# Performance work log

Measured on AMD Instinct MI355X. Metric: run time of the kernel, lower is better.

## Reference

```python
import jax, jax.numpy as jnp
import numpy as np

D_MODEL = 768
CTX_DIM = 1024
N_HEAD = 12
N_QUERIES = 256
DIM_HEAD = D_MODEL // N_HEAD  # 64
INNER = DIM_HEAD * N_HEAD     # 768
EPS = 1e-5


def layernorm(x, w, b):
    mu = jnp.mean(x, axis=-1, keepdims=True)
    var = jnp.mean((x - mu) ** 2, axis=-1, keepdims=True)
    return (x - mu) * jax.lax.rsqrt(var + EPS) * w + b


def setup_inputs() -> dict:
    key = jax.random.key(0)
    ks = jax.random.split(key, 9)
    x = jax.random.normal(ks[0], (8, 4096, CTX_DIM), dtype=jnp.float32)
    query = jax.random.normal(ks[1], (N_QUERIES, D_MODEL), dtype=jnp.float32)
    # Linear weights stored [in, out] (y = x @ W)
    Wq = jax.random.normal(ks[2], (D_MODEL, INNER), dtype=jnp.float32) * 0.02
    Wkv = jax.random.normal(ks[3], (CTX_DIM, 2 * INNER), dtype=jnp.float32) * 0.02
    Wout = jax.random.normal(ks[4], (INNER, D_MODEL), dtype=jnp.float32) * 0.02
    ln_q_w = jnp.ones((D_MODEL,), jnp.float32)
    ln_q_b = jnp.zeros((D_MODEL,), jnp.float32)
    ln_k_w = jnp.ones((CTX_DIM,), jnp.float32)
    ln_k_b = jnp.zeros((CTX_DIM,), jnp.float32)
    return {"x": x, "query": query, "ln_q_w": ln_q_w, "ln_q_b": ln_q_b,
            "ln_k_w": ln_k_w, "ln_k_b": ln_k_b, "Wq": Wq, "Wkv": Wkv, "Wout": Wout}


def reference(x, query, ln_q_w, ln_q_b, ln_k_w, ln_k_b, Wq, Wkv, Wout):
    b = x.shape[0]
    h, dh = N_HEAD, DIM_HEAD
    scale = dh ** -0.5
    xk = x[:, None]  # b 1 n d  (m = 1)
    m, n = xk.shape[1], xk.shape[2]
    q = jnp.broadcast_to(query, (b, m) + query.shape)  # b m nq d
    xk = layernorm(xk, ln_k_w, ln_k_b)
    q = layernorm(q, ln_q_w, ln_q_b)
    q = q @ Wq                          # b m nq inner
    kv = xk @ Wkv                       # b m n 2*inner
    k, v = jnp.split(kv, 2, axis=-1)
    def split_heads(t):
        bb, tt, nn, _ = t.shape
        return t.reshape(bb, tt, nn, h, dh).transpose(0, 3, 1, 2, 4)  # b h t n dh
    q, k, v = split_heads(q), split_heads(k), split_heads(v)
    sim = jnp.einsum('bhtid,bhtjd->bhtij', q * scale, k)
    attn = jax.nn.softmax(sim, axis=-1)
    out = jnp.einsum('bhtij,bhtjd->bhtid', attn, v)  # b h t nq dh
    out = out.transpose(0, 2, 3, 1, 4).reshape(b, m, N_QUERIES, INNER)
    return (out @ Wout).squeeze(axis=1)  # b nq d_model
```

## Files before the change

### kernel.cpp

```cpp
#include <hip/hip_runtime.h>
#include <hip/hip_bf16.h>
#include <math.h>

#define B_    8
#define T_    4096
#define CD    1024
#define DM    768
#define NH    12
#define DH    64
#define NQ    256
#define INNER 768
#define NKV   1536
#define MKV   (B_*T_)
#define EPS   1e-5f
#define SCALE 0.125f

typedef __attribute__((ext_vector_type(8))) short short8;
typedef __attribute__((ext_vector_type(4))) float f32x4;

__device__ __forceinline__ unsigned short f2bf(float f) {
  union { __hip_bfloat16 h; unsigned short u; } cv;
  cv.h = __float2bfloat16(f);
  return cv.u;
}

__global__ __launch_bounds__(256) void tb32_kernel(
    const float* __restrict__ src, unsigned short* __restrict__ dst,
    int Cn, int R) {
  __shared__ float tile[32][33];
  int k0 = blockIdx.x * 32, n0 = blockIdx.y * 32;
  int tid = threadIdx.x;
  int r = tid >> 3, c4 = (tid & 7) * 4;
  float4 v = *reinterpret_cast<const float4*>(&src[(size_t)(k0 + r) * Cn + n0 + c4]);
  tile[r][c4 + 0] = v.x; tile[r][c4 + 1] = v.y; tile[r][c4 + 2] = v.z; tile[r][c4 + 3] = v.w;
  __syncthreads();
  ushort4 o4;
  o4.x = f2bf(tile[c4 + 0][r]);
  o4.y = f2bf(tile[c4 + 1][r]);
  o4.z = f2bf(tile[c4 + 2][r]);
  o4.w = f2bf(tile[c4 + 3][r]);
  *reinterpret_cast<ushort4*>(&dst[(size_t)(n0 + r) * R + k0 + c4]) = o4;
}

__global__ __launch_bounds__(256) void qln_kernel(
    const float* __restrict__ query, const float* __restrict__ lnw,
    const float* __restrict__ lnb, unsigned short* __restrict__ qn) {
  int row = blockIdx.x, tid = threadIdx.x;
  __shared__ float rbuf[256];
  const float* qr = query + (size_t)row * DM;
  float v0 = qr[tid], v1 = qr[tid + 256], v2 = qr[tid + 512];
  rbuf[tid] = v0 + v1 + v2;
  __syncthreads();
  for (int o = 128; o > 0; o >>= 1) { if (tid < o) rbuf[tid] += rbuf[tid + o]; __syncthreads(); }
  float mean = rbuf[0] * (1.f / 768.f);
  __syncthreads();
  float d0 = v0 - mean, d1 = v1 - mean, d2 = v2 - mean;
  rbuf[tid] = d0 * d0 + d1 * d1 + d2 * d2;
  __syncthreads();
  for (int o = 128; o > 0; o >>= 1) { if (tid < o) rbuf[tid] += rbuf[tid + o]; __syncthreads(); }
  float var = rbuf[0] * (1.f / 768.f);
  float rs = rsqrtf(var + EPS);
  unsigned short* dst = qn + (size_t)row * DM;
  dst[tid]       = f2bf(d0 * rs * lnw[tid]       + lnb[tid]);
  dst[tid + 256] = f2bf(d1 * rs * lnw[tid + 256] + lnb[tid + 256]);
  dst[tid + 512] = f2bf(d2 * rs * lnw[tid + 512] + lnb[tid + 512]);
}

__global__ __launch_bounds__(256) void xnorm_kernel(
    const float* __restrict__ x, const float* __restrict__ lnw,
    const float* __restrict__ lnb, unsigned short* __restrict__ xn) {
  int row = blockIdx.x, tid = threadIdx.x;
  float4 v = reinterpret_cast<const float4*>(x + (size_t)row * CD)[tid];
  float s  = v.x + v.y + v.z + v.w;
  float ss = v.x * v.x + v.y * v.y + v.z * v.z + v.w * v.w;
  #pragma unroll
  for (int o = 32; o > 0; o >>= 1) { s += __shfl_down(s, o); ss += __shfl_down(ss, o); }
  __shared__ float sm[8];
  int wid = tid >> 6, lane = tid & 63;
  if (lane == 0) { sm[wid] = s; sm[4 + wid] = ss; }
  __syncthreads();
  float S  = sm[0] + sm[1] + sm[2] + sm[3];
  float SS = sm[4] + sm[5] + sm[6] + sm[7];
  float m  = S * (1.f / 1024.f);
  float var = SS * (1.f / 1024.f) - m * m;
  float rs = rsqrtf(fmaxf(var, 0.f) + EPS);
  float4 wv = reinterpret_cast<const float4*>(lnw)[tid];
  float4 bv = reinterpret_cast<const float4*>(lnb)[tid];
  ushort4 o4;
  o4.x = f2bf((v.x - m) * rs * wv.x + bv.x);
  o4.y = f2bf((v.y - m) * rs * wv.y + bv.y);
  o4.z = f2bf((v.z - m) * rs * wv.z + bv.z);
  o4.w = f2bf((v.w - m) * rs * wv.w + bv.w);
  reinterpret_cast<ushort4*>(xn + (size_t)row * CD)[tid] = o4;
}

template <int MODE>
__global__ __launch_bounds__(256) void gemm128_kernel(
    const unsigned short* __restrict__ A, const unsigned short* __restrict__ Bt,
    void* __restrict__ Cout, int N, int K, int nN, float scale, int swz) {
  __shared__ __attribute__((aligned(16))) unsigned short As[128 * 64];
  __shared__ __attribute__((aligned(16))) unsigned short Bs[128 * 64];
  int tid = threadIdx.x;
  int w = tid >> 6, lane = tid & 63;
  int bid = blockIdx.x;
  int sw = swz ? ((bid & 7) * ((int)gridDim.x >> 3) + (bid >> 3)) : bid;
  int mt = sw / nN, nt = sw % nN;
  int m0 = mt * 128, n0 = nt * 128;

  int srow[4], skoff[4];
  #pragma unroll
  for (int i = 0; i < 4; ++i) {
    int L = w * 4096 + i * 1024 + lane * 16;
    int row = L >> 7;
    int slot = (L >> 4) & 7;
    srow[i] = row;
    skoff[i] = ((slot ^ (row & 7)) << 3);
  }

  f32x4 acc[4][4];
  #pragma unroll
  for (int m = 0; m < 4; ++m)
    #pragma unroll
    for (int n = 0; n < 4; ++n) acc[m][n] = (f32x4){0.f, 0.f, 0.f, 0.f};

  int wr = w >> 1, wc = w & 1;
  int l15 = lane & 15, l4 = lane >> 4;

  for (int t = 0; t < K / 64; ++t) {
    int k0 = t * 64;
    #pragma unroll
    for (int i = 0; i < 4; ++i) {
      __builtin_amdgcn_global_load_lds(
          (const __attribute__((address_space(1))) void*)(A + (size_t)(m0 + srow[i]) * K + k0 + skoff[i]),
          (__attribute__((address_space(3))) void*)(As + w * 2048 + i * 512 + lane * 8),
          16, 0, 0);
    }
    #pragma unroll
    for (int i = 0; i < 4; ++i) {
      __builtin_amdgcn_global_load_lds(
          (const __attribute__((address_space(1))) void*)(Bt + (size_t)(n0 + srow[i]) * K + k0 + skoff[i]),
          (__attribute__((address_space(3))) void*)(Bs + w * 2048 + i * 512 + lane * 8),
          16, 0, 0);
    }
    __syncthreads();
    #pragma unroll
    for (int kh = 0; kh < 2; ++kh) {
      short8 af[4], bf[4];
      #pragma unroll
      for (int m = 0; m < 4; ++m) {
        int row = wr * 64 + m * 16 + l15;
        int byte = row * 128 + (((l4 + 4 * kh) ^ (row & 7)) << 4);
        af[m] = *reinterpret_cast<const short8*>(reinterpret_cast<const char*>(As) + byte);
      }
      #pragma unroll
      for (int n = 0; n < 4; ++n) {
        int row = wc * 64 + n * 16 + l15;
        int byte = row * 128 + (((l4 + 4 * kh) ^ (row & 7)) << 4);
        bf[n] = *reinterpret_cast<const short8*>(reinterpret_cast<const char*>(Bs) + byte);
      }
      #pragma unroll
      for (int m = 0; m < 4; ++m)
        #pragma unroll
        for (int n = 0; n < 4; ++n)
          acc[m][n] = __builtin_amdgcn_mfma_f32_16x16x32_bf16(af[m], bf[n], acc[m][n], 0, 0, 0);
    }
    __syncthreads();
  }

  #pragma unroll
  for (int m = 0; m < 4; ++m) {
    int grow = m0 + wr * 64 + m * 16 + l4 * 4;
    #pragma unroll
    for (int n = 0; n < 4; ++n) {
      int gcol = n0 + wc * 64 + n * 16 + l15;
      #pragma unroll
      for (int r = 0; r < 4; ++r) {
        if (MODE == 0)
          ((unsigned short*)Cout)[(size_t)(grow + r) * N + gcol] = f2bf(acc[m][n][r] * scale);
        else
          ((float*)Cout)[(size_t)(grow + r) * N + gcol] = acc[m][n][r];
      }
    }
  }
}

#define KBM 256
#define KBN 256
#define KBK 64
__global__ __launch_bounds__(512, 2) void kv_mfma256_kernel(
    const unsigned short* __restrict__ xn, const unsigned short* __restrict__ wkvT,
    unsigned short* __restrict__ kvb) {
  __shared__ __attribute__((aligned(16))) unsigned short As[2][KBM * KBK];
  __shared__ __attribute__((aligned(16))) unsigned short Bs[2][KBN * KBK];
  int tid = threadIdx.x;
  int w = tid >> 6, lane = tid & 63;
  int wm = w >> 2, wn = w & 3;
  int l15 = lane & 15, l4 = lane >> 4;

  int bid = blockIdx.x;
  int sw = (bid & 7) * 96 + (bid >> 3);
  int mt = sw / (NKV / KBN), nt = sw % (NKV / KBN);
  int m0 = mt * KBM, n0 = nt * KBN;

  int srow[4], koff[4];
  #pragma unroll
  for (int i = 0; i < 4; ++i) {
    int r = i * 64 + (tid >> 3);
    srow[i] = r;
    koff[i] = (((tid & 7) ^ (r & 7)) << 3);
  }

  f32x4 acc[8][4];
  #pragma unroll
  for (int m = 0; m < 8; ++m)
    #pragma unroll
    for (int n = 0; n < 4; ++n) acc[m][n] = (f32x4){0.f, 0.f, 0.f, 0.f};

  #pragma unroll
  for (int i = 0; i < 4; ++i) {
    __builtin_amdgcn_global_load_lds(
        (const __attribute__((address_space(1))) void*)(xn + (size_t)(m0 + srow[i]) * CD + koff[i]),
        (__attribute__((address_space(3))) void*)(&As[0][0] + i * 4096 + tid * 8), 16, 0, 0);
    __builtin_amdgcn_global_load_lds(
        (const __attribute__((address_space(1))) void*)(wkvT + (size_t)(n0 + srow[i]) * CD + koff[i]),
        (__attribute__((address_space(3))) void*)(&Bs[0][0] + i * 4096 + tid * 8), 16, 0, 0);
  }
  __syncthreads();

  for (int t = 0; t < CD / KBK; ++t) {
    int cur = t & 1;
    if (t + 1 < CD / KBK) {
      int k0 = (t + 1) * KBK;
      #pragma unroll
      for (int i = 0; i < 4; ++i) {
        __builtin_amdgcn_global_load_lds(
            (const __attribute__((address_space(1))) void*)(xn + (size_t)(m0 + srow[i]) * CD + k0 + koff[i]),
            (__attribute__((address_space(3))) void*)(&As[cur ^ 1][0] + i * 4096 + tid * 8), 16, 0, 0);
        __builtin_amdgcn_global_load_lds(
            (const __attribute__((address_space(1))) void*)(wkvT + (size_t)(n0 + srow[i]) * CD + k0 + koff[i]),
            (__attribute__((address_space(3))) void*)(&Bs[cur ^ 1][0] + i * 4096 + tid * 8), 16, 0, 0);
      }
    }
    const char* Ab = reinterpret_cast<const char*>(&As[cur][0]);
    const char* Bb = reinterpret_cast<const char*>(&Bs[cur][0]);
    #pragma unroll
    for (int kh = 0; kh < 2; ++kh) {
      short8 bf[4];
      #pragma unroll
      for (int n = 0; n < 4; ++n) {
        int row = wn * 64 + n * 16 + l15;
        int byt = row * 128 + (((kh * 4 + l4) ^ (row & 7)) << 4);
        bf[n] = *reinterpret_cast<const short8*>(Bb + byt);
      }
      #pragma unroll
      for (int m = 0; m < 8; ++m) {
        int row = wm * 128 + m * 16 + l15;
        int byt = row * 128 + (((kh * 4 + l4) ^ (row & 7)) << 4);
        short8 af = *reinterpret_cast<const short8*>(Ab + byt);
        #pragma unroll
        for (int n = 0; n < 4; ++n)
          acc[m][n] = __builtin_amdgcn_mfma_f32_16x16x32_bf16(af, bf[n], acc[m][n], 0, 0, 0);
      }
    }
    __syncthreads();
  }

  #pragma unroll
  for (int m = 0; m < 8; ++m) {
    int grow = m0 + wm * 128 + m * 16 + l4 * 4;
    #pragma unroll
    for (int n = 0; n < 4; ++n) {
      int gcol = n0 + wn * 64 + n * 16 + l15;
      #pragma unroll
      for (int r = 0; r < 4; ++r)
        kvb[(size_t)(grow + r) * NKV + gcol] = f2bf(acc[m][n][r]);
    }
  }
}

__global__ __launch_bounds__(256) void vtrans_kernel(
    const unsigned short* __restrict__ kvb, unsigned short* __restrict__ vT) {
  int jt = blockIdx.x, bh = blockIdx.y;
  int b = bh / NH, h = bh % NH;
  __shared__ __attribute__((aligned(16))) unsigned short t_[64][72];
  int tid = threadIdx.x;
  {
    int jr = tid >> 2, dp = (tid & 3) * 16;
    const unsigned short* src = kvb + (size_t)(b * T_ + jt * 64 + jr) * NKV + INNER + h * DH + dp;
    *reinterpret_cast<short8*>(&t_[jr][dp])     = *reinterpret_cast<const short8*>(src);
    *reinterpret_cast<short8*>(&t_[jr][dp + 8]) = *reinterpret_cast<const short8*>(src + 8);
  }
  __syncthreads();
  {
    int d = tid >> 2, jp = (tid & 3) * 16;
    unsigned short tmp[16];
    #pragma unroll
    for (int jj = 0; jj < 16; ++jj) tmp[jj] = t_[jp + jj][d];
    unsigned short* dst = vT + ((size_t)bh * DH + d) * T_ + jt * 64 + jp;
    *reinterpret_cast<short8*>(dst)     = *reinterpret_cast<const short8*>(&tmp[0]);
    *reinterpret_cast<short8*>(dst + 8) = *reinterpret_cast<const short8*>(&tmp[8]);
  }
}

__global__ __launch_bounds__(256) void attn_mfma_kernel(
    const unsigned short* __restrict__ qpb, const unsigned short* __restrict__ kvb,
    const unsigned short* __restrict__ vT,
    float* __restrict__ pO, float* __restrict__ pM, float* __restrict__ pL) {
  int qt = blockIdx.x, kc = blockIdx.y, bh = blockIdx.z;
  int b = bh / NH, h = bh % NH;
  __shared__ __attribute__((aligned(16))) unsigned short Ks[4096];
  __shared__ __attribute__((aligned(16))) unsigned short Vs[4096];
  __shared__ __attribute__((aligned(16))) unsigned short Ps[4][1024];
  int tid = threadIdx.x;
  int w = tid >> 6, lane = tid & 63;
  int l15 = lane & 15, l4 = lane >> 4;

  short8 qf[2];
  {
    const unsigned short* qb = qpb + (size_t)(qt * 64 + w * 16 + l15) * INNER + h * DH;
    qf[0] = *reinterpret_cast<const short8*>(qb + l4 * 8);
    qf[1] = *reinterpret_cast<const short8*>(qb + 32 + l4 * 8);
  }

  int srow0 = w * 16 + (lane >> 3);
  int srow1 = srow0 + 8;
  int koff0 = (((lane & 7) ^ (srow0 & 7)) << 3);
  int koff1 = (((lane & 7) ^ (srow1 & 7)) << 3);

  f32x4 o[4];
  #pragma unroll
  for (int i = 0; i < 4; ++i) o[i] = (f32x4){0.f, 0.f, 0.f, 0.f};
  float m_run = -1e30f, l_run = 0.f;

  const size_t kbase = ((size_t)b * T_) * NKV + h * DH;
  const size_t vbase = ((size_t)bh * DH) * T_;

  for (int kt = 0; kt < 32; ++kt) {
    int j0 = kc * 2048 + kt * 64;
    __builtin_amdgcn_global_load_lds(
        (const __attribute__((address_space(1))) void*)(kvb + kbase + (size_t)(j0 + srow0) * NKV + koff0),
        (__attribute__((address_space(3))) void*)(Ks + w * 1024 + lane * 8), 16, 0, 0);
    __builtin_amdgcn_global_load_lds(
        (const __attribute__((address_space(1))) void*)(kvb + kbase + (size_t)(j0 + srow1) * NKV + koff1),
        (__attribute__((address_space(3))) void*)(Ks + w * 1024 + 512 + lane * 8), 16, 0, 0);
    __builtin_amdgcn_global_load_lds(
        (const __attribute__((address_space(1))) void*)(vT + vbase + (size_t)srow0 * T_ + j0 + koff0),
        (__attribute__((address_space(3))) void*)(Vs + w * 1024 + lane * 8), 16, 0, 0);
    __builtin_amdgcn_global_load_lds(
        (const __attribute__((address_space(1))) void*)(vT + vbase + (size_t)srow1 * T_ + j0 + koff1),
        (__attribute__((address_space(3))) void*)(Vs + w * 1024 + 512 + lane * 8), 16, 0, 0);
    __syncthreads();

    f32x4 st[4];
    #pragma unroll
    for (int sub = 0; sub < 4; ++sub) {
      st[sub] = (f32x4){0.f, 0.f, 0.f, 0.f};
      #pragma unroll
      for (int hf = 0; hf < 2; ++hf) {
        int row = sub * 16 + l15;
        int byt = row * 128 + (((l4 + 4 * hf) ^ (row & 7)) << 4);
        short8 kf = *reinterpret_cast<const short8*>(reinterpret_cast<const char*>(Ks) + byt);
        st[sub] = __builtin_amdgcn_mfma_f32_16x16x32_bf16(kf, qf[hf], st[sub], 0, 0, 0);
      }
    }

    float tmax = -1e30f;
    #pragma unroll
    for (int sub = 0; sub < 4; ++sub)
      #pragma unroll
      for (int r = 0; r < 4; ++r) tmax = fmaxf(tmax, st[sub][r]);
    tmax = fmaxf(tmax, __shfl_xor(tmax, 16));
    tmax = fmaxf(tmax, __shfl_xor(tmax, 32));
    float m_new = fmaxf(m_run, tmax);
    float alpha = __expf(m_run - m_new);
    float psum = 0.f;
    #pragma unroll
    for (int sub = 0; sub < 4; ++sub) {
      float p0 = __expf(st[sub][0] - m_new);
      float p1 = __expf(st[sub][1] - m_new);
      float p2 = __expf(st[sub][2] - m_new);
      float p3 = __expf(st[sub][3] - m_new);
      psum += (p0 + p1) + (p2 + p3);
      unsigned int u0 = (unsigned int)f2bf(p0) | ((unsigned int)f2bf(p1) << 16);
      unsigned int u1 = (unsigned int)f2bf(p2) | ((unsigned int)f2bf(p3) << 16);
      int slot = (sub * 2 + (l4 >> 1)) ^ (l15 & 7);
      int byt = l15 * 128 + (slot << 4) + (l4 & 1) * 8;
      uint2 uv; uv.x = u0; uv.y = u1;
      *reinterpret_cast<uint2*>(reinterpret_cast<char*>(Ps[w]) + byt) = uv;
    }
    psum += __shfl_xor(psum, 16);
    psum += __shfl_xor(psum, 32);
    l_run = l_run * alpha + psum;
    m_run = m_new;

    float ao[4];
    #pragma unroll
    for (int r = 0; r < 4; ++r) ao[r] = __shfl(alpha, (l4 << 2) | r);
    #pragma unroll
    for (int ds = 0; ds < 4; ++ds)
      #pragma unroll
      for (int r = 0; r < 4; ++r) o[ds][r] *= ao[r];

    short8 pa[2];
    #pragma unroll
    for (int hf = 0; hf < 2; ++hf) {
      int byt = l15 * 128 + ((((hf << 2) + l4) ^ (l15 & 7)) << 4);
      pa[hf] = *reinterpret_cast<const short8*>(reinterpret_cast<const char*>(Ps[w]) + byt);
    }
    #pragma unroll
    for (int ds = 0; ds < 4; ++ds) {
      #pragma unroll
      for (int hf = 0; hf < 2; ++hf) {
        int row = ds * 16 + l15;
        int byt = row * 128 + (((l4 + 4 * hf) ^ (row & 7)) << 4);
        short8 vf = *reinterpret_cast<const short8*>(reinterpret_cast<const char*>(Vs) + byt);
        o[ds] = __builtin_amdgcn_mfma_f32_16x16x32_bf16(pa[hf], vf, o[ds], 0, 0, 0);
      }
    }
    __syncthreads();
  }

  int pidx = bh * 2 + kc;
  int qrow0 = qt * 64 + w * 16;
  if (l4 == 0) {
    pM[(size_t)pidx * NQ + qrow0 + l15] = m_run;
    pL[(size_t)pidx * NQ + qrow0 + l15] = l_run;
  }
  #pragma unroll
  for (int ds = 0; ds < 4; ++ds)
    #pragma unroll
    for (int r = 0; r < 4; ++r)
      pO[((size_t)pidx * NQ + qrow0 + l4 * 4 + r) * DH + ds * 16 + l15] = o[ds][r];
}

__global__ __launch_bounds__(256) void attn_combine_kernel(
    const float* __restrict__ pO, const float* __restrict__ pM,
    const float* __restrict__ pL, unsigned short* __restrict__ attn_out) {
  int qt = blockIdx.x, bh = blockIdx.y;
  int b = bh / NH, h = bh % NH;
  int tid = threadIdx.x;
  #pragma unroll
  for (int e = 0; e < 16; ++e) {
    int idx = e * 256 + tid;
    int r = idx >> 6, d = idx & 63;
    int row = qt * 64 + r;
    size_t i0 = (size_t)(bh * 2 + 0) * NQ + row;
    size_t i1 = (size_t)(bh * 2 + 1) * NQ + row;
    float m1 = pM[i0], m2 = pM[i1], l1 = pL[i0], l2 = pL[i1];
    float M = fmaxf(m1, m2);
    float w1 = __expf(m1 - M), w2 = __expf(m2 - M);
    float L = l1 * w1 + l2 * w2;
    float oo = (pO[i0 * DH + d] * w1 + pO[i1 * DH + d] * w2) / L;
    attn_out[((size_t)b * NQ + row) * INNER + h * DH + d] = f2bf(oo);
  }
}

extern "C" void kernel_launch(void* const* d_in, const int* in_sizes, int n_in,
                              void* d_out, int out_size, void* d_ws, size_t ws_size,
                              hipStream_t stream) {
  const float* x      = (const float*)d_in[0];
  const float* query  = (const float*)d_in[1];
  const float* ln_q_w = (const float*)d_in[2];
  const float* ln_q_b = (const float*)d_in[3];
  const float* ln_k_w = (const float*)d_in[4];
  const float* ln_k_b = (const float*)d_in[5];
  const float* Wq     = (const float*)d_in[6];
  const float* Wkv    = (const float*)d_in[7];
  const float* Wout   = (const float*)d_in[8];
  float* out = (float*)d_out;

  unsigned short* qpb   = (unsigned short*)d_ws;
  unsigned short* xn    = qpb + (size_t)NQ * INNER;
  unsigned short* vT    = xn;
  unsigned short* wkvT  = xn + (size_t)MKV * CD;
  unsigned short* kvb   = wkvT + (size_t)NKV * CD;
  float* pO    = (float*)(kvb + (size_t)MKV * NKV);
  float* pM    = pO + (size_t)B_ * NH * 2 * NQ * DH;
  float* pL    = pM + (size_t)B_ * NH * 2 * NQ;
  unsigned short* attnb = (unsigned short*)(pL + (size_t)B_ * NH * 2 * NQ);
  unsigned short* qn    = attnb + (size_t)B_ * NQ * INNER;
  unsigned short* WqT   = qn + (size_t)NQ * DM;
  unsigned short* WoutT = WqT + (size_t)DM * INNER;

  hipLaunchKernelGGL(tb32_kernel, dim3(CD / 32, NKV / 32), dim3(256), 0, stream,
                     Wkv, wkvT, NKV, CD);
  hipLaunchKernelGGL(tb32_kernel, dim3(DM / 32, INNER / 32), dim3(256), 0, stream,
                     Wq, WqT, INNER, DM);
  hipLaunchKernelGGL(tb32_kernel, dim3(INNER / 32, DM / 32), dim3(256), 0, stream,
                     Wout, WoutT, DM, INNER);
  hipLaunchKernelGGL(qln_kernel, dim3(NQ), dim3(256), 0, stream,
                     query, ln_q_w, ln_q_b, qn);
  hipLaunchKernelGGL((gemm128_kernel<0>), dim3((NQ / 128) * (INNER / 128)), dim3(256), 0, stream,
                     qn, WqT, (void*)qpb, INNER, DM, INNER / 128, SCALE, 0);
  hipLaunchKernelGGL(xnorm_kernel, dim3(MKV), dim3(256), 0, stream,
                     x, ln_k_w, ln_k_b, xn);
  hipLaunchKernelGGL(kv_mfma256_kernel, dim3((MKV / KBM) * (NKV / KBN)), dim3(512), 0, stream,
                     xn, wkvT, kvb);
  hipLaunchKernelGGL(vtrans_kernel, dim3(T_ / 64, B_ * NH), dim3(256), 0, stream,
                     kvb, vT);
  hipLaunchKernelGGL(attn_mfma_kernel, dim3(4, 2, B_ * NH), dim3(256), 0, stream,
                     qpb, kvb, vT, pO, pM, pL);
  hipLaunchKernelGGL(attn_combine_kernel, dim3(4, B_ * NH), dim3(256), 0, stream,
                     pO, pM, pL, attnb);
  hipLaunchKernelGGL((gemm128_kernel<1>), dim3((B_ * NQ / 128) * (DM / 128)), dim3(256), 0, stream,
                     attnb, WoutT, (void*)out, DM, INNER, DM / 128, 1.f, 1);
}
```

Baseline: 284.8 us.

## Restructure KV GEMM into quadrant-phased 8-wave pipeline with split staging

Rewrites the KV projection GEMM so each K-step is split into four MFMA quadrants. Each half-tile of A and B is staged separately and interleaved between the quadrants, with fine-grained vmcnt waits and s_barriers. The goal is to overlap global-to-LDS loads with MFMA work and raise MFMA issue priority with s_setprio, replacing the single whole-tile prefetch plus __syncthreads. setprio is also added around the MFMA blocks in the attention kernel. The many extra barriers and the tighter hand scheduling risk stalls, and the vmcnt counting could be fragile.

```diff
diff --git a/kernel.cpp b/kernel.cpp
--- a/kernel.cpp
+++ b/kernel.cpp
@@ -187,11 +187,31 @@
 #define KBM 256
 #define KBN 256
 #define KBK 64
-__global__ __launch_bounds__(512, 2) void kv_mfma256_kernel(
+#define NT  (CD / KBK)
+
+#define QUAD(qm, qn)                                                          \
+  do {                                                                        \
+    __builtin_amdgcn_s_setprio(1);                                            \
+    _Pragma("unroll")                                                         \
+    for (int m_ = 0; m_ < 4; ++m_) {                                          \
+      _Pragma("unroll")                                                       \
+      for (int n_ = 0; n_ < 2; ++n_) {                                        \
+        acc[(qm)*4 + m_][(qn)*2 + n_] = __builtin_amdgcn_mfma_f32_16x16x32_bf16( \
+            areg[(qm)*4 + m_][0], breg[(qn)*2 + n_][0],                       \
+            acc[(qm)*4 + m_][(qn)*2 + n_], 0, 0, 0);                          \
+        acc[(qm)*4 + m_][(qn)*2 + n_] = __builtin_amdgcn_mfma_f32_16x16x32_bf16( \
+            areg[(qm)*4 + m_][1], breg[(qn)*2 + n_][1],                       \
+            acc[(qm)*4 + m_][(qn)*2 + n_], 0, 0, 0);                          \
+      }                                                                       \
+    }                                                                         \
+    __builtin_amdgcn_s_setprio(0);                                            \
+  } while (0)
+
+__global__ __launch_bounds__(512, 2) void kv_mfma8p_kernel(
     const unsigned short* __restrict__ xn, const unsigned short* __restrict__ wkvT,
     unsigned short* __restrict__ kvb) {
-  __shared__ __attribute__((aligned(16))) unsigned short As[2][KBM * KBK];
-  __shared__ __attribute__((aligned(16))) unsigned short Bs[2][KBN * KBK];
+  __shared__ __attribute__((aligned(16))) unsigned short AsL[2][2][128 * 64];
+  __shared__ __attribute__((aligned(16))) unsigned short BsL[2][2][128 * 64];
   int tid = threadIdx.x;
   int w = tid >> 6, lane = tid & 63;
   int wm = w >> 2, wn = w & 3;
@@ -202,13 +222,31 @@
   int mt = sw / (NKV / KBN), nt = sw % (NKV / KBN);
   int m0 = mt * KBM, n0 = nt * KBN;
 
-  int srow[4], koff[4];
-  #pragma unroll
-  for (int i = 0; i < 4; ++i) {
-    int r = i * 64 + (tid >> 3);
-    srow[i] = r;
-    koff[i] = (((tid & 7) ^ (r & 7)) << 3);
-  }
+  int sr0 = tid >> 3;
+  int sr1 = 64 + (tid >> 3);
+  int sk0 = ((tid & 7) ^ (sr0 & 7)) << 3;
+  int sk1 = ((tid & 7) ^ (sr1 & 7)) << 3;
+
+  auto stageA = [&](int t, int h) {
+    int d = t & 1;
+    const unsigned short* src = xn + (size_t)(m0 + h * 128) * CD + t * KBK;
+    __builtin_amdgcn_global_load_lds(
+        (const __attribute__((address_space(1))) void*)(src + (size_t)sr0 * CD + sk0),
+        (__attribute__((address_space(3))) void*)(&AsL[d][h][0] + tid * 8), 16, 0, 0);
+    __builtin_amdgcn_global_load_lds(
+        (const __attribute__((address_space(1))) void*)(src + (size_t)sr1 * CD + sk1),
+        (__attribute__((address_space(3))) void*)(&AsL[d][h][4096] + tid * 8), 16, 0, 0);
+  };
+  auto stageB = [&](int t, int h) {
+    int d = t & 1;
+    const unsigned short* src = wkvT + (size_t)(n0 + h * 128) * CD + t * KBK;
+    __builtin_amdgcn_global_load_lds(
+        (const __attribute__((address_space(1))) void*)(src + (size_t)sr0 * CD + sk0),
+        (__attribute__((address_space(3))) void*)(&BsL[d][h][0] + tid * 8), 16, 0, 0);
+    __builtin_amdgcn_global_load_lds(
+        (const __attribute__((address_space(1))) void*)(src + (size_t)sr1 * CD + sk1),
+        (__attribute__((address_space(3))) void*)(&BsL[d][h][4096] + tid * 8), 16, 0, 0);
+  };
 
   f32x4 acc[8][4];
   #pragma unroll
@@ -216,53 +254,56 @@
     #pragma unroll
     for (int n = 0; n < 4; ++n) acc[m][n] = (f32x4){0.f, 0.f, 0.f, 0.f};
 
-  #pragma unroll
-  for (int i = 0; i < 4; ++i) {
-    __builtin_amdgcn_global_load_lds(
-        (const __attribute__((address_space(1))) void*)(xn + (size_t)(m0 + srow[i]) * CD + koff[i]),
-        (__attribute__((address_space(3))) void*)(&As[0][0] + i * 4096 + tid * 8), 16, 0, 0);
-    __builtin_amdgcn_global_load_lds(
-        (const __attribute__((address_space(1))) void*)(wkvT + (size_t)(n0 + srow[i]) * CD + koff[i]),
-        (__attribute__((address_space(3))) void*)(&Bs[0][0] + i * 4096 + tid * 8), 16, 0, 0);
-  }
-  __syncthreads();
-
-  for (int t = 0; t < CD / KBK; ++t) {
-    int cur = t & 1;
-    if (t + 1 < CD / KBK) {
-      int k0 = (t + 1) * KBK;
-      #pragma unroll
-      for (int i = 0; i < 4; ++i) {
-        __builtin_amdgcn_global_load_lds(
-            (const __attribute__((address_space(1))) void*)(xn + (size_t)(m0 + srow[i]) * CD + k0 + koff[i]),
-            (__attribute__((address_space(3))) void*)(&As[cur ^ 1][0] + i * 4096 + tid * 8), 16, 0, 0);
-        __builtin_amdgcn_global_load_lds(
-            (const __attribute__((address_space(1))) void*)(wkvT + (size_t)(n0 + srow[i]) * CD + k0 + koff[i]),
-            (__attribute__((address_space(3))) void*)(&Bs[cur ^ 1][0] + i * 4096 + tid * 8), 16, 0, 0);
-      }
-    }
-    const char* Ab = reinterpret_cast<const char*>(&As[cur][0]);
-    const char* Bb = reinterpret_cast<const char*>(&Bs[cur][0]);
-    #pragma unroll
-    for (int kh = 0; kh < 2; ++kh) {
-      short8 bf[4];
-      #pragma unroll
-      for (int n = 0; n < 4; ++n) {
-        int row = wn * 64 + n * 16 + l15;
-        int byt = row * 128 + (((kh * 4 + l4) ^ (row & 7)) << 4);
-        bf[n] = *reinterpret_cast<const short8*>(Bb + byt);
-      }
-      #pragma unroll
-      for (int m = 0; m < 8; ++m) {
-        int row = wm * 128 + m * 16 + l15;
-        int byt = row * 128 + (((kh * 4 + l4) ^ (row & 7)) << 4);
-        short8 af = *reinterpret_cast<const short8*>(Ab + byt);
-        #pragma unroll
-        for (int n = 0; n < 4; ++n)
-          acc[m][n] = __builtin_amdgcn_mfma_f32_16x16x32_bf16(af, bf[n], acc[m][n], 0, 0, 0);
-      }
-    }
-    __syncthreads();
+  short8 areg[8][2], breg[4][2];
+
+  auto rdA = [&](int t, int m, int kh) -> short8 {
+    int row = m * 16 + l15;
+    int byt = row * 128 + (((kh * 4 + l4) ^ (row & 7)) << 4);
+    return *reinterpret_cast<const short8*>(
+        reinterpret_cast<const char*>(&AsL[t & 1][wm][0]) + byt);
+  };
+  auto rdB = [&](int t, int n, int kh) -> short8 {
+    int R = wn * 64 + n * 16 + l15;
+    int row = R & 127;
+    int byt = row * 128 + (((kh * 4 + l4) ^ (row & 7)) << 4);
+    return *reinterpret_cast<const short8*>(
+        reinterpret_cast<const char*>(&BsL[t & 1][R >> 7][0]) + byt);
+  };
+
+  stageA(0, 0); stageA(0, 1); stageB(0, 0); stageB(0, 1);
+
+  for (int t = 0; t < NT; ++t) {
+    if (t < NT - 1) {
+      stageA(t + 1, 0);
+      asm volatile("s_waitcnt vmcnt(2)" ::: "memory");
+    } else {
+      asm volatile("s_waitcnt vmcnt(0)" ::: "memory");
+    }
+    __builtin_amdgcn_s_barrier();
+    __builtin_amdgcn_sched_barrier(0);
+    #pragma unroll
+    for (int m = 0; m < 4; ++m) { areg[m][0] = rdA(t, m, 0); areg[m][1] = rdA(t, m, 1); }
+    #pragma unroll
+    for (int n = 0; n < 2; ++n) { breg[n][0] = rdB(t, n, 0); breg[n][1] = rdB(t, n, 1); }
+    QUAD(0, 0);
+    __builtin_amdgcn_s_barrier();
+    if (t < NT - 1) stageA(t + 1, 1);
+    #pragma unroll
+    for (int m = 4; m < 8; ++m) { areg[m][0] = rdA(t, m, 0); areg[m][1] = rdA(t, m, 1); }
+    __builtin_amdgcn_s_barrier();
+    QUAD(1, 0);
+    __builtin_amdgcn_s_barrier();
+    if (t < NT - 1) stageB(t + 1, 0);
+    #pragma unroll
+    for (int n = 2; n < 4; ++n) { breg[n][0] = rdB(t, n, 0); breg[n][1] = rdB(t, n, 1); }
+    __builtin_amdgcn_s_barrier();
+    QUAD(1, 1);
+    __builtin_amdgcn_s_barrier();
+    if (t < NT - 1) stageB(t + 1, 1);
+    __builtin_amdgcn_s_barrier();
+    QUAD(0, 1);
+    __builtin_amdgcn_s_barrier();
+    __builtin_amdgcn_sched_barrier(0);
   }
 
   #pragma unroll
@@ -352,6 +393,7 @@
     __syncthreads();
 
     f32x4 st[4];
+    __builtin_amdgcn_s_setprio(1);
     #pragma unroll
     for (int sub = 0; sub < 4; ++sub) {
       st[sub] = (f32x4){0.f, 0.f, 0.f, 0.f};
@@ -363,6 +405,7 @@
         st[sub] = __builtin_amdgcn_mfma_f32_16x16x32_bf16(kf, qf[hf], st[sub], 0, 0, 0);
       }
     }
+    __builtin_amdgcn_s_setprio(0);
 
     float tmax = -1e30f;
     #pragma unroll
@@ -407,6 +450,7 @@
       int byt = l15 * 128 + ((((hf << 2) + l4) ^ (l15 & 7)) << 4);
       pa[hf] = *reinterpret_cast<const short8*>(reinterpret_cast<const char*>(Ps[w]) + byt);
     }
+    __builtin_amdgcn_s_setprio(1);
     #pragma unroll
     for (int ds = 0; ds < 4; ++ds) {
       #pragma unroll
@@ -417,6 +461,7 @@
         o[ds] = __builtin_amdgcn_mfma_f32_16x16x32_bf16(pa[hf], vf, o[ds], 0, 0, 0);
       }
     }
+    __builtin_amdgcn_s_setprio(0);
     __syncthreads();
   }
 
@@ -494,7 +539,7 @@
                      qn, WqT, (void*)qpb, INNER, DM, INNER / 128, SCALE, 0);
   hipLaunchKernelGGL(xnorm_kernel, dim3(MKV), dim3(256), 0, stream,
                      x, ln_k_w, ln_k_b, xn);
-  hipLaunchKernelGGL(kv_mfma256_kernel, dim3((MKV / KBM) * (NKV / KBN)), dim3(512), 0, stream,
+  hipLaunchKernelGGL(kv_mfma8p_kernel, dim3((MKV / KBM) * (NKV / KBN)), dim3(512), 0, stream,
                      xn, wkvT, kvb);
   hipLaunchKernelGGL(vtrans_kernel, dim3(T_ / 64, B_ * NH), dim3(256), 0, stream,
                      kvb, vT);
```

Result: slower. 314.3 us (+10.4%).

## Use 4-stage LDS ring in KV GEMM and double-buffer K/V in attention

Applied to the files above, without the earlier changes.

The KV projection GEMM moves from a double-buffered K=64 tile to a four-slot ring of K=32 tiles, with three stages prefetched. It waits with explicit vmcnt counts and raw s_barrier, and raises wave priority around the MFMA block. The attention kernel double-buffers its K/V LDS tiles so the next tile's global_load_lds overlaps the current compute instead of stalling on a full sync. The goal is to hide global memory latency behind MFMA work. The hand-written waitcnt counts depend on the exact number of outstanding loads, which is fragile, and the smaller K step doubles barrier frequency in the GEMM.

```diff
diff --git a/kernel.cpp b/kernel.cpp
--- a/kernel.cpp
+++ b/kernel.cpp
@@ -186,12 +186,14 @@
 
 #define KBM 256
 #define KBN 256
-#define KBK 64
-__global__ __launch_bounds__(512, 2) void kv_mfma256_kernel(
+#define RBK 32
+#define RNT (CD / RBK)
+
+__global__ __launch_bounds__(512, 2) void kv_ring_kernel(
     const unsigned short* __restrict__ xn, const unsigned short* __restrict__ wkvT,
     unsigned short* __restrict__ kvb) {
-  __shared__ __attribute__((aligned(16))) unsigned short As[2][KBM * KBK];
-  __shared__ __attribute__((aligned(16))) unsigned short Bs[2][KBN * KBK];
+  __shared__ __attribute__((aligned(16))) unsigned short As[4][KBM * RBK];
+  __shared__ __attribute__((aligned(16))) unsigned short Bs[4][KBN * RBK];
   int tid = threadIdx.x;
   int w = tid >> 6, lane = tid & 63;
   int wm = w >> 2, wn = w & 3;
@@ -202,13 +204,28 @@
   int mt = sw / (NKV / KBN), nt = sw % (NKV / KBN);
   int m0 = mt * KBM, n0 = nt * KBN;
 
-  int srow[4], koff[4];
-  #pragma unroll
-  for (int i = 0; i < 4; ++i) {
-    int r = i * 64 + (tid >> 3);
-    srow[i] = r;
-    koff[i] = (((tid & 7) ^ (r & 7)) << 3);
-  }
+  int sr0 = tid >> 2;
+  int sr1 = 128 + (tid >> 2);
+  int sk0 = ((tid & 3) ^ (sr0 & 3)) << 3;
+  int sk1 = ((tid & 3) ^ (sr1 & 3)) << 3;
+
+  auto stage = [&](int t) {
+    int s = t & 3;
+    const unsigned short* sa = xn + (size_t)m0 * CD + t * RBK;
+    const unsigned short* sb = wkvT + (size_t)n0 * CD + t * RBK;
+    __builtin_amdgcn_global_load_lds(
+        (const __attribute__((address_space(1))) void*)(sa + (size_t)sr0 * CD + sk0),
+        (__attribute__((address_space(3))) void*)(&As[s][0] + tid * 8), 16, 0, 0);
+    __builtin_amdgcn_global_load_lds(
+        (const __attribute__((address_space(1))) void*)(sa + (size_t)sr1 * CD + sk1),
+        (__attribute__((address_space(3))) void*)(&As[s][4096] + tid * 8), 16, 0, 0);
+    __builtin_amdgcn_global_load_lds(
+        (const __attribute__((address_space(1))) void*)(sb + (size_t)sr0 * CD + sk0),
+        (__attribute__((address_space(3))) void*)(&Bs[s][0] + tid * 8), 16, 0, 0);
+    __builtin_amdgcn_global_load_lds(
+        (const __attribute__((address_space(1))) void*)(sb + (size_t)sr1 * CD + sk1),
+        (__attribute__((address_space(3))) void*)(&Bs[s][4096] + tid * 8), 16, 0, 0);
+  };
 
   f32x4 acc[8][4];
   #pragma unroll
@@ -216,53 +233,38 @@
     #pragma unroll
     for (int n = 0; n < 4; ++n) acc[m][n] = (f32x4){0.f, 0.f, 0.f, 0.f};
 
-  #pragma unroll
-  for (int i = 0; i < 4; ++i) {
-    __builtin_amdgcn_global_load_lds(
-        (const __attribute__((address_space(1))) void*)(xn + (size_t)(m0 + srow[i]) * CD + koff[i]),
-        (__attribute__((address_space(3))) void*)(&As[0][0] + i * 4096 + tid * 8), 16, 0, 0);
-    __builtin_amdgcn_global_load_lds(
-        (const __attribute__((address_space(1))) void*)(wkvT + (size_t)(n0 + srow[i]) * CD + koff[i]),
-        (__attribute__((address_space(3))) void*)(&Bs[0][0] + i * 4096 + tid * 8), 16, 0, 0);
-  }
-  __syncthreads();
-
-  for (int t = 0; t < CD / KBK; ++t) {
-    int cur = t & 1;
-    if (t + 1 < CD / KBK) {
-      int k0 = (t + 1) * KBK;
-      #pragma unroll
-      for (int i = 0; i < 4; ++i) {
-        __builtin_amdgcn_global_load_lds(
-            (const __attribute__((address_space(1))) void*)(xn + (size_t)(m0 + srow[i]) * CD + k0 + koff[i]),
-            (__attribute__((address_space(3))) void*)(&As[cur ^ 1][0] + i * 4096 + tid * 8), 16, 0, 0);
-        __builtin_amdgcn_global_load_lds(
-            (const __attribute__((address_space(1))) void*)(wkvT + (size_t)(n0 + srow[i]) * CD + k0 + koff[i]),
-            (__attribute__((address_space(3))) void*)(&Bs[cur ^ 1][0] + i * 4096 + tid * 8), 16, 0, 0);
-      }
-    }
-    const char* Ab = reinterpret_cast<const char*>(&As[cur][0]);
-    const char* Bb = reinterpret_cast<const char*>(&Bs[cur][0]);
-    #pragma unroll
-    for (int kh = 0; kh < 2; ++kh) {
-      short8 bf[4];
-      #pragma unroll
-      for (int n = 0; n < 4; ++n) {
-        int row = wn * 64 + n * 16 + l15;
-        int byt = row * 128 + (((kh * 4 + l4) ^ (row & 7)) << 4);
-        bf[n] = *reinterpret_cast<const short8*>(Bb + byt);
-      }
-      #pragma unroll
-      for (int m = 0; m < 8; ++m) {
-        int row = wm * 128 + m * 16 + l15;
-        int byt = row * 128 + (((kh * 4 + l4) ^ (row & 7)) << 4);
-        short8 af = *reinterpret_cast<const short8*>(Ab + byt);
-        #pragma unroll
-        for (int n = 0; n < 4; ++n)
-          acc[m][n] = __builtin_amdgcn_mfma_f32_16x16x32_bf16(af, bf[n], acc[m][n], 0, 0, 0);
-      }
-    }
-    __syncthreads();
+  stage(0); stage(1); stage(2);
+
+  for (int t = 0; t < RNT; ++t) {
+    if (t + 3 < RNT) stage(t + 3);
+    if (t < RNT - 2)       asm volatile("s_waitcnt vmcnt(8)" ::: "memory");
+    else if (t == RNT - 2) asm volatile("s_waitcnt vmcnt(4)" ::: "memory");
+    else                   asm volatile("s_waitcnt vmcnt(0)" ::: "memory");
+    __builtin_amdgcn_s_barrier();
+    __builtin_amdgcn_sched_barrier(0);
+
+    const char* Ab = reinterpret_cast<const char*>(&As[t & 3][0]);
+    const char* Bb = reinterpret_cast<const char*>(&Bs[t & 3][0]);
+    short8 areg[8], breg[4];
+    #pragma unroll
+    for (int n = 0; n < 4; ++n) {
+      int row = wn * 64 + n * 16 + l15;
+      breg[n] = *reinterpret_cast<const short8*>(Bb + row * 64 + ((l4 ^ (row & 3)) << 4));
+    }
+    #pragma unroll
+    for (int m = 0; m < 8; ++m) {
+      int row = wm * 128 + m * 16 + l15;
+      areg[m] = *reinterpret_cast<const short8*>(Ab + row * 64 + ((l4 ^ (row & 3)) << 4));
+    }
+    __builtin_amdgcn_s_setprio(1);
+    #pragma unroll
+    for (int m = 0; m < 8; ++m)
+      #pragma unroll
+      for (int n = 0; n < 4; ++n)
+        acc[m][n] = __builtin_amdgcn_mfma_f32_16x16x32_bf16(areg[m], breg[n], acc[m][n], 0, 0, 0);
+    __builtin_amdgcn_s_setprio(0);
+    __builtin_amdgcn_s_barrier();
+    __builtin_amdgcn_sched_barrier(0);
   }
 
   #pragma unroll
@@ -308,8 +310,8 @@
     float* __restrict__ pO, float* __restrict__ pM, float* __restrict__ pL) {
   int qt = blockIdx.x, kc = blockIdx.y, bh = blockIdx.z;
   int b = bh / NH, h = bh % NH;
-  __shared__ __attribute__((aligned(16))) unsigned short Ks[4096];
-  __shared__ __attribute__((aligned(16))) unsigned short Vs[4096];
+  __shared__ __attribute__((aligned(16))) unsigned short Ks[2][4096];
+  __shared__ __attribute__((aligned(16))) unsigned short Vs[2][4096];
   __shared__ __attribute__((aligned(16))) unsigned short Ps[4][1024];
   int tid = threadIdx.x;
   int w = tid >> 6, lane = tid & 63;
@@ -327,31 +329,48 @@
   int koff0 = (((lane & 7) ^ (srow0 & 7)) << 3);
   int koff1 = (((lane & 7) ^ (srow1 & 7)) << 3);
 
+  const size_t kbase = ((size_t)b * T_) * NKV + h * DH;
+  const size_t vbase = ((size_t)bh * DH) * T_;
+
+  auto stageKV = [&](int kt, int d) {
+    int j0 = kc * 2048 + kt * 64;
+    __builtin_amdgcn_global_load_lds(
+        (const __attribute__((address_space(1))) void*)(kvb + kbase + (size_t)(j0 + srow0) * NKV + koff0),
+        (__attribute__((address_space(3))) void*)(&Ks[d][0] + w * 1024 + lane * 8), 16, 0, 0);
+    __builtin_amdgcn_global_load_lds(
+        (const __attribute__((address_space(1))) void*)(kvb + kbase + (size_t)(j0 + srow1) * NKV + koff1),
+        (__attribute__((address_space(3))) void*)(&Ks[d][0] + w * 1024 + 512 + lane * 8), 16, 0, 0);
+    __builtin_amdgcn_global_load_lds(
+        (const __attribute__((address_space(1))) void*)(vT + vbase + (size_t)srow0 * T_ + j0 + koff0),
+        (__attribute__((address_space(3))) void*)(&Vs[d][0] + w * 1024 + lane * 8), 16, 0, 0);
+    __builtin_amdgcn_global_load_lds(
+        (const __attribute__((address_space(1))) void*)(vT + vbase + (size_t)srow1 * T_ + j0 + koff1),
+        (__attribute__((address_space(3))) void*)(&Vs[d][0] + w * 1024 + 512 + lane * 8), 16, 0, 0);
+  };
+
   f32x4 o[4];
   #pragma unroll
   for (int i = 0; i < 4; ++i) o[i] = (f32x4){0.f, 0.f, 0.f, 0.f};
   float m_run = -1e30f, l_run = 0.f;
 
-  const size_t kbase = ((size_t)b * T_) * NKV + h * DH;
-  const size_t vbase = ((size_t)bh * DH) * T_;
+  stageKV(0, 0);
 
   for (int kt = 0; kt < 32; ++kt) {
-    int j0 = kc * 2048 + kt * 64;
-    __builtin_amdgcn_global_load_lds(
-        (const __attribute__((address_space(1))) void*)(kvb + kbase + (size_t)(j0 + srow0) * NKV + koff0),
-        (__attribute__((address_space(3))) void*)(Ks + w * 1024 + lane * 8), 16, 0, 0);
-    __builtin_amdgcn_global_load_lds(
-        (const __attribute__((address_space(1))) void*)(kvb + kbase + (size_t)(j0 + srow1) * NKV + koff1),
-        (__attribute__((address_space(3))) void*)(Ks + w * 1024 + 512 + lane * 8), 16, 0, 0);
-    __builtin_amdgcn_global_load_lds(
-        (const __attribute__((address_space(1))) void*)(vT + vbase + (size_t)srow0 * T_ + j0 + koff0),
-        (__attribute__((address_space(3))) void*)(Vs + w * 1024 + lane * 8), 16, 0, 0);
-    __builtin_amdgcn_global_load_lds(
-        (const __attribute__((address_space(1))) void*)(vT + vbase + (size_t)srow1 * T_ + j0 + koff1),
-        (__attribute__((address_space(3))) void*)(Vs + w * 1024 + 512 + lane * 8), 16, 0, 0);
-    __syncthreads();
+    int cur = kt & 1;
+    if (kt + 1 < 32) {
+      stageKV(kt + 1, cur ^ 1);
+      asm volatile("s_waitcnt vmcnt(4)" ::: "memory");
+    } else {
+      asm volatile("s_waitcnt vmcnt(0)" ::: "memory");
+    }
+    __builtin_amdgcn_s_barrier();
+    __builtin_amdgcn_sched_barrier(0);
+
+    const char* Kb = reinterpret_cast<const char*>(&Ks[cur][0]);
+    const char* Vb = reinterpret_cast<const char*>(&Vs[cur][0]);
 
     f32x4 st[4];
+    __builtin_amdgcn_s_setprio(1);
     #pragma unroll
     for (int sub = 0; sub < 4; ++sub) {
       st[sub] = (f32x4){0.f, 0.f, 0.f, 0.f};
@@ -359,10 +378,11 @@
       for (int hf = 0; hf < 2; ++hf) {
         int row = sub * 16 + l15;
         int byt = row * 128 + (((l4 + 4 * hf) ^ (row & 7)) << 4);
-        short8 kf = *reinterpret_cast<const short8*>(reinterpret_cast<const char*>(Ks) + byt);
+        short8 kf = *reinterpret_cast<const short8*>(Kb + byt);
         st[sub] = __builtin_amdgcn_mfma_f32_16x16x32_bf16(kf, qf[hf], st[sub], 0, 0, 0);
       }
     }
+    __builtin_amdgcn_s_setprio(0);
 
     float tmax = -1e30f;
     #pragma unroll
@@ -407,17 +427,20 @@
       int byt = l15 * 128 + ((((hf << 2) + l4) ^ (l15 & 7)) << 4);
       pa[hf] = *reinterpret_cast<const short8*>(reinterpret_cast<const char*>(Ps[w]) + byt);
     }
+    __builtin_amdgcn_s_setprio(1);
     #pragma unroll
     for (int ds = 0; ds < 4; ++ds) {
       #pragma unroll
       for (int hf = 0; hf < 2; ++hf) {
         int row = ds * 16 + l15;
         int byt = row * 128 + (((l4 + 4 * hf) ^ (row & 7)) << 4);
-        short8 vf = *reinterpret_cast<const short8*>(reinterpret_cast<const char*>(Vs) + byt);
+        short8 vf = *reinterpret_cast<const short8*>(Vb + byt);
         o[ds] = __builtin_amdgcn_mfma_f32_16x16x32_bf16(pa[hf], vf, o[ds], 0, 0, 0);
       }
     }
-    __syncthreads();
+    __builtin_amdgcn_s_setprio(0);
+    __builtin_amdgcn_s_barrier();
+    __builtin_amdgcn_sched_barrier(0);
   }
 
   int pidx = bh * 2 + kc;
@@ -494,7 +517,7 @@
                      qn, WqT, (void*)qpb, INNER, DM, INNER / 128, SCALE, 0);
   hipLaunchKernelGGL(xnorm_kernel, dim3(MKV), dim3(256), 0, stream,
                      x, ln_k_w, ln_k_b, xn);
-  hipLaunchKernelGGL(kv_mfma256_kernel, dim3((MKV / KBM) * (NKV / KBN)), dim3(512), 0, stream,
+  hipLaunchKernelGGL(kv_ring_kernel, dim3((MKV / KBM) * (NKV / KBN)), dim3(512), 0, stream,
                      xn, wkvT, kvb);
   hipLaunchKernelGGL(vtrans_kernel, dim3(T_ / 64, B_ * NH), dim3(256), 0, stream,
                      kvb, vT);
```

Result: slower. 307.8 us (+8.1%).

## Fuse V transpose into KV GEMM epilogue and double-buffer attention K/V loads

Applied to the files above, without the earlier changes.

The KV projection epilogue now writes K to its own compact buffer and writes V straight into transposed per-head layout, which removes the separate vtrans kernel and its extra read and write of V. The attention kernel double-buffers K/V tiles in LDS and prefetches the next tile with explicit vmcnt waits and raw barriers, adding s_setprio around the MFMA sections. The transposed V stores are 8-byte strided writes, which may coalesce poorly, and the doubled LDS use may lower attention occupancy.

```diff
diff --git a/kernel.cpp b/kernel.cpp
--- a/kernel.cpp
+++ b/kernel.cpp
@@ -187,9 +187,9 @@
 #define KBM 256
 #define KBN 256
 #define KBK 64
-__global__ __launch_bounds__(512, 2) void kv_mfma256_kernel(
+__global__ __launch_bounds__(512, 2) void kv_split_kernel(
     const unsigned short* __restrict__ xn, const unsigned short* __restrict__ wkvT,
-    unsigned short* __restrict__ kvb) {
+    unsigned short* __restrict__ kvbK, unsigned short* __restrict__ vT) {
   __shared__ __attribute__((aligned(16))) unsigned short As[2][KBM * KBK];
   __shared__ __attribute__((aligned(16))) unsigned short Bs[2][KBN * KBK];
   int tid = threadIdx.x;
@@ -265,51 +265,44 @@
     __syncthreads();
   }
 
-  #pragma unroll
-  for (int m = 0; m < 8; ++m) {
-    int grow = m0 + wm * 128 + m * 16 + l4 * 4;
-    #pragma unroll
-    for (int n = 0; n < 4; ++n) {
-      int gcol = n0 + wn * 64 + n * 16 + l15;
-      #pragma unroll
-      for (int r = 0; r < 4; ++r)
-        kvb[(size_t)(grow + r) * NKV + gcol] = f2bf(acc[m][n][r]);
-    }
-  }
-}
-
-__global__ __launch_bounds__(256) void vtrans_kernel(
-    const unsigned short* __restrict__ kvb, unsigned short* __restrict__ vT) {
-  int jt = blockIdx.x, bh = blockIdx.y;
-  int b = bh / NH, h = bh % NH;
-  __shared__ __attribute__((aligned(16))) unsigned short t_[64][72];
-  int tid = threadIdx.x;
-  {
-    int jr = tid >> 2, dp = (tid & 3) * 16;
-    const unsigned short* src = kvb + (size_t)(b * T_ + jt * 64 + jr) * NKV + INNER + h * DH + dp;
-    *reinterpret_cast<short8*>(&t_[jr][dp])     = *reinterpret_cast<const short8*>(src);
-    *reinterpret_cast<short8*>(&t_[jr][dp + 8]) = *reinterpret_cast<const short8*>(src + 8);
-  }
-  __syncthreads();
-  {
-    int d = tid >> 2, jp = (tid & 3) * 16;
-    unsigned short tmp[16];
-    #pragma unroll
-    for (int jj = 0; jj < 16; ++jj) tmp[jj] = t_[jp + jj][d];
-    unsigned short* dst = vT + ((size_t)bh * DH + d) * T_ + jt * 64 + jp;
-    *reinterpret_cast<short8*>(dst)     = *reinterpret_cast<const short8*>(&tmp[0]);
-    *reinterpret_cast<short8*>(dst + 8) = *reinterpret_cast<const short8*>(&tmp[8]);
+  if (nt < 3) {
+    #pragma unroll
+    for (int m = 0; m < 8; ++m) {
+      int grow = m0 + wm * 128 + m * 16 + l4 * 4;
+      #pragma unroll
+      for (int n = 0; n < 4; ++n) {
+        int gcol = nt * 256 + wn * 64 + n * 16 + l15;
+        #pragma unroll
+        for (int r = 0; r < 4; ++r)
+          kvbK[(size_t)(grow + r) * INNER + gcol] = f2bf(acc[m][n][r]);
+      }
+    }
+  } else {
+    int b = m0 >> 12;
+    int h = (nt - 3) * 4 + wn;
+    #pragma unroll
+    for (int m = 0; m < 8; ++m) {
+      int j = (m0 & 4095) + wm * 128 + m * 16 + l4 * 4;
+      #pragma unroll
+      for (int n = 0; n < 4; ++n) {
+        int d = n * 16 + l15;
+        ushort4 o4;
+        o4.x = f2bf(acc[m][n][0]); o4.y = f2bf(acc[m][n][1]);
+        o4.z = f2bf(acc[m][n][2]); o4.w = f2bf(acc[m][n][3]);
+        *reinterpret_cast<ushort4*>(&vT[((size_t)(b * NH + h) * DH + d) * T_ + j]) = o4;
+      }
+    }
   }
 }
 
 __global__ __launch_bounds__(256) void attn_mfma_kernel(
-    const unsigned short* __restrict__ qpb, const unsigned short* __restrict__ kvb,
+    const unsigned short* __restrict__ qpb, const unsigned short* __restrict__ kvbK,
     const unsigned short* __restrict__ vT,
     float* __restrict__ pO, float* __restrict__ pM, float* __restrict__ pL) {
   int qt = blockIdx.x, kc = blockIdx.y, bh = blockIdx.z;
   int b = bh / NH, h = bh % NH;
-  __shared__ __attribute__((aligned(16))) unsigned short Ks[4096];
-  __shared__ __attribute__((aligned(16))) unsigned short Vs[4096];
+  __shared__ __attribute__((aligned(16))) unsigned short Ks[2][4096];
+  __shared__ __attribute__((aligned(16))) unsigned short Vs[2][4096];
   __shared__ __attribute__((aligned(16))) unsigned short Ps[4][1024];
   int tid = threadIdx.x;
   int w = tid >> 6, lane = tid & 63;
@@ -327,31 +320,48 @@
   int koff0 = (((lane & 7) ^ (srow0 & 7)) << 3);
   int koff1 = (((lane & 7) ^ (srow1 & 7)) << 3);
 
+  const size_t kbase = ((size_t)b * T_) * INNER + h * DH;
+  const size_t vbase = ((size_t)bh * DH) * T_;
+
+  auto stageKV = [&](int kt, int d) {
+    int j0 = kc * 2048 + kt * 64;
+    __builtin_amdgcn_global_load_lds(
+        (const __attribute__((address_space(1))) void*)(kvbK + kbase + (size_t)(j0 + srow0) * INNER + koff0),
+        (__attribute__((address_space(3))) void*)(&Ks[d][0] + w * 1024 + lane * 8), 16, 0, 0);
+    __builtin_amdgcn_global_load_lds(
+        (const __attribute__((address_space(1))) void*)(kvbK + kbase + (size_t)(j0 + srow1) * INNER + koff1),
+        (__attribute__((address_space(3))) void*)(&Ks[d][0] + w * 1024 + 512 + lane * 8), 16, 0, 0);
+    __builtin_amdgcn_global_load_lds(
+        (const __attribute__((address_space(1))) void*)(vT + vbase + (size_t)srow0 * T_ + j0 + koff0),
+        (__attribute__((address_space(3))) void*)(&Vs[d][0] + w * 1024 + lane * 8), 16, 0, 0);
+    __builtin_amdgcn_global_load_lds(
+        (const __attribute__((address_space(1))) void*)(vT + vbase + (size_t)srow1 * T_ + j0 + koff1),
+        (__attribute__((address_space(3))) void*)(&Vs[d][0] + w * 1024 + 512 + lane * 8), 16, 0, 0);
+  };
+
   f32x4 o[4];
   #pragma unroll
   for (int i = 0; i < 4; ++i) o[i] = (f32x4){0.f, 0.f, 0.f, 0.f};
   float m_run = -1e30f, l_run = 0.f;
 
-  const size_t kbase = ((size_t)b * T_) * NKV + h * DH;
-  const size_t vbase = ((size_t)bh * DH) * T_;
+  stageKV(0, 0);
 
   for (int kt = 0; kt < 32; ++kt) {
-    int j0 = kc * 2048 + kt * 64;
-    __builtin_amdgcn_global_load_lds(
-        (const __attribute__((address_space(1))) void*)(kvb + kbase + (size_t)(j0 + srow0) * NKV + koff0),
-        (__attribute__((address_space(3))) void*)(Ks + w * 1024 + lane * 8), 16, 0, 0);
-    __builtin_amdgcn_global_load_lds(
-        (const __attribute__((address_space(1))) void*)(kvb + kbase + (size_t)(j0 + srow1) * NKV + koff1),
-        (__attribute__((address_space(3))) void*)(Ks + w * 1024 + 512 + lane * 8), 16, 0, 0);
-    __builtin_amdgcn_global_load_lds(
-        (const __attribute__((address_space(1))) void*)(vT + vbase + (size_t)srow0 * T_ + j0 + koff0),
-        (__attribute__((address_space(3))) void*)(Vs + w * 1024 + lane * 8), 16, 0, 0);
-    __builtin_amdgcn_global_load_lds(
-        (const __attribute__((address_space(1))) void*)(vT + vbase + (size_t)srow1 * T_ + j0 + koff1),
-        (__attribute__((address_space(3))) void*)(Vs + w * 1024 + 512 + lane * 8), 16, 0, 0);
-    __syncthreads();
+    int cur = kt & 1;
+    if (kt + 1 < 32) {
+      stageKV(kt + 1, cur ^ 1);
+      asm volatile("s_waitcnt vmcnt(4)" ::: "memory");
+    } else {
+      asm volatile("s_waitcnt vmcnt(0)" ::: "memory");
+    }
+    __builtin_amdgcn_s_barrier();
+    __builtin_amdgcn_sched_barrier(0);
+
+    const char* Kb = reinterpret_cast<const char*>(&Ks[cur][0]);
+    const char* Vb = reinterpret_cast<const char*>(&Vs[cur][0]);
 
     f32x4 st[4];
+    __builtin_amdgcn_s_setprio(1);
     #pragma unroll
     for (int sub = 0; sub < 4; ++sub) {
       st[sub] = (f32x4){0.f, 0.f, 0.f, 0.f};
@@ -359,10 +369,11 @@
       for (int hf = 0; hf < 2; ++hf) {
         int row = sub * 16 + l15;
         int byt = row * 128 + (((l4 + 4 * hf) ^ (row & 7)) << 4);
-        short8 kf = *reinterpret_cast<const short8*>(reinterpret_cast<const char*>(Ks) + byt);
+        short8 kf = *reinterpret_cast<const short8*>(Kb + byt);
         st[sub] = __builtin_amdgcn_mfma_f32_16x16x32_bf16(kf, qf[hf], st[sub], 0, 0, 0);
       }
     }
+    __builtin_amdgcn_s_setprio(0);
 
     float tmax = -1e30f;
     #pragma unroll
@@ -407,17 +418,20 @@
       int byt = l15 * 128 + ((((hf << 2) + l4) ^ (l15 & 7)) << 4);
       pa[hf] = *reinterpret_cast<const short8*>(reinterpret_cast<const char*>(Ps[w]) + byt);
     }
+    __builtin_amdgcn_s_setprio(1);
     #pragma unroll
     for (int ds = 0; ds < 4; ++ds) {
       #pragma unroll
       for (int hf = 0; hf < 2; ++hf) {
         int row = ds * 16 + l15;
         int byt = row * 128 + (((l4 + 4 * hf) ^ (row & 7)) << 4);
-        short8 vf = *reinterpret_cast<const short8*>(reinterpret_cast<const char*>(Vs) + byt);
+        short8 vf = *reinterpret_cast<const short8*>(Vb + byt);
         o[ds] = __builtin_amdgcn_mfma_f32_16x16x32_bf16(pa[hf], vf, o[ds], 0, 0, 0);
       }
     }
-    __syncthreads();
+    __builtin_amdgcn_s_setprio(0);
+    __builtin_amdgcn_s_barrier();
+    __builtin_amdgcn_sched_barrier(0);
   }
 
   int pidx = bh * 2 + kc;
@@ -471,10 +485,10 @@
 
   unsigned short* qpb   = (unsigned short*)d_ws;
   unsigned short* xn    = qpb + (size_t)NQ * INNER;
-  unsigned short* vT    = xn;
   unsigned short* wkvT  = xn + (size_t)MKV * CD;
-  unsigned short* kvb   = wkvT + (size_t)NKV * CD;
-  float* pO    = (float*)(kvb + (size_t)MKV * NKV);
+  unsigned short* kvbK  = wkvT + (size_t)NKV * CD;
+  unsigned short* vT    = kvbK + (size_t)MKV * INNER;
+  float* pO    = (float*)(vT + (size_t)MKV * INNER);
   float* pM    = pO + (size_t)B_ * NH * 2 * NQ * DH;
   float* pL    = pM + (size_t)B_ * NH * 2 * NQ;
   unsigned short* attnb = (unsigned short*)(pL + (size_t)B_ * NH * 2 * NQ);
@@ -494,12 +508,10 @@
                      qn, WqT, (void*)qpb, INNER, DM, INNER / 128, SCALE, 0);
   hipLaunchKernelGGL(xnorm_kernel, dim3(MKV), dim3(256), 0, stream,
                      x, ln_k_w, ln_k_b, xn);
-  hipLaunchKernelGGL(kv_mfma256_kernel, dim3((MKV / KBM) * (NKV / KBN)), dim3(512), 0, stream,
-                     xn, wkvT, kvb);
-  hipLaunchKernelGGL(vtrans_kernel, dim3(T_ / 64, B_ * NH), dim3(256), 0, stream,
-                     kvb, vT);
+  hipLaunchKernelGGL(kv_split_kernel, dim3((MKV / KBM) * (NKV / KBN)), dim3(512), 0, stream,
+                     xn, wkvT, kvbK, vT);
   hipLaunchKernelGGL(attn_mfma_kernel, dim3(4, 2, B_ * NH), dim3(256), 0, stream,
-                     qpb, kvb, vT, pO, pM, pL);
+                     qpb, kvbK, vT, pO, pM, pL);
   hipLaunchKernelGGL(attn_combine_kernel, dim3(4, B_ * NH), dim3(256), 0, stream,
                      pO, pM, pL, attnb);
   hipLaunchKernelGGL((gemm128_kernel<1>), dim3((B_ * NQ / 128) * (DM / 128)), dim3(256), 0, stream,
```

New measurement: 275.4 us. -3.3%, faster.
